# Optimization experiments

Measured on AMD Instinct MI355X. Metric: run time of the kernel, lower is better.

Reference implementation:

```python
import jax, jax.numpy as jnp
import numpy as np

B, H, N, C = 4, 16, 1024, 64
D = H * C  # d_model = 1024


def setup_inputs() -> dict:
    key = jax.random.key(0)
    ks = jax.random.split(key, 6)
    q = jax.random.normal(ks[0], (B, H, N, C), dtype=jnp.float32)
    k = jax.random.normal(ks[1], (B, H, N, C), dtype=jnp.float32)
    v = jax.random.normal(ks[2], (B, H, N, C), dtype=jnp.float32)
    pe = jax.random.normal(ks[3], (1, H, N, N), dtype=jnp.float32)
    # Mlp(h*c): fc1 D->D, SiLU, fc2 D->D (stored as [in, out] for x @ W)
    w1 = jax.random.normal(ks[4], (D, D), dtype=jnp.float32) * (D ** -0.5)
    b1 = jnp.zeros((D,), dtype=jnp.float32)
    w2 = jax.random.normal(ks[5], (D, D), dtype=jnp.float32) * (D ** -0.5)
    b2 = jnp.zeros((D,), dtype=jnp.float32)
    return {"q": q, "k": k, "v": v, "pe": pe,
            "w1": w1, "b1": b1, "w2": w2, "b2": b2}


def reference(q, k, v, pe, w1, b1, w2, b2):
    b, h, n, c = q.shape
    scale = c ** (-0.5)
    # scores: [b,h,n,n]; softmax FIRST, then add pe bias (post-softmax bias)
    scores = jnp.einsum('bhnc,bhmc->bhnm', q, k) * scale
    attn = pe + jax.nn.softmax(scores, axis=-1)
    ctx = jnp.einsum('bhnm,bhmc->bhnc', attn, v)
    # [b,h,n,c] -> [b,n,h*c]
    out = ctx.transpose(0, 2, 1, 3).reshape(b, n, h * c)
    # Mlp: fc1 -> SiLU -> fc2 (dropout is identity at eval)
    hdn = jax.nn.silu(out @ w1 + b1)
    return hdn @ w2 + b2
```

## Files before the change

kernel.cpp:

```cpp
#include <hip/hip_runtime.h>

#define B_ 4
#define H_ 16
#define N_ 1024
#define C_ 64
#define D_ 1024

typedef _Float16 half8 __attribute__((ext_vector_type(8)));
typedef _Float16 half4v __attribute__((ext_vector_type(4)));
typedef float f32x4 __attribute__((ext_vector_type(4)));
typedef float f32x16 __attribute__((ext_vector_type(16)));
typedef unsigned int uint4v __attribute__((ext_vector_type(4)));

#define MFMA16(a, b, c) __builtin_amdgcn_mfma_f32_16x16x32_f16(a, b, c, 0, 0, 0)
#define MFMA32(a, b, c) __builtin_amdgcn_mfma_f32_32x32x16_f16(a, b, c, 0, 0, 0)
#define SM_SHIFT 6.0f

static __device__ __forceinline__ unsigned pk2(float a, float b) {
  auto h = __builtin_amdgcn_cvt_pkrtz(a, b);
  return __builtin_bit_cast(unsigned, h);
}
static __device__ __forceinline__ void swap32(unsigned& a, unsigned& b) {
  asm volatile("v_permlane32_swap_b32 %0, %1" : "+v"(a), "+v"(b));
}
static __device__ __forceinline__ void gload16(const void* g, void* l) {
  __builtin_amdgcn_global_load_lds(
      (const __attribute__((address_space(1))) unsigned int*)g,
      (__attribute__((address_space(3))) unsigned int*)l, 16, 0, 0);
}

__global__ __launch_bounds__(256) void transpose_cvt(
    const float* __restrict__ in, _Float16* __restrict__ outp,
    int in_stride, int out_stride, long in_bstride, long out_bstride)
{
  __shared__ float t[64][65];
  const int tid = threadIdx.x;
  const int r0 = blockIdx.x * 64, c0 = blockIdx.y * 64;
  const float* inb = in + (size_t)blockIdx.z * in_bstride;
  _Float16* outb = outp + (size_t)blockIdx.z * out_bstride;
#pragma unroll
  for (int i = 0; i < 4; ++i) {
    int idx = i * 256 + tid;
    int r = idx >> 4, c4 = (idx & 15) << 2;
    float4 a = *(const float4*)(inb + (size_t)(r0 + r) * in_stride + c0 + c4);
    t[r][c4] = a.x; t[r][c4 + 1] = a.y; t[r][c4 + 2] = a.z; t[r][c4 + 3] = a.w;
  }
  __syncthreads();
#pragma unroll
  for (int i = 0; i < 2; ++i) {
    int idx = i * 256 + tid;
    int rr = idx >> 3, c8 = (idx & 7) << 3;
    half8 hv;
#pragma unroll
    for (int j = 0; j < 8; ++j) hv[j] = (_Float16)t[c8 + j][rr];
    *(half8*)(outb + (size_t)(c0 + rr) * out_stride + r0 + c8) = hv;
  }
}

__global__ __launch_bounds__(512, 1) void pev_kernel(
    const float* __restrict__ pe, const _Float16* __restrict__ vth,
    _Float16* __restrict__ xpe)
{
  __shared__ __align__(16) _Float16 a_lds[2][64][72];
  __shared__ __align__(16) _Float16 b_lds[2][256][72];
  const int tid = threadIdx.x;
  const int n0 = blockIdx.x * 64;
  const int h = blockIdx.y;
  const float* peb = pe + (size_t)h * N_ * N_ + (size_t)n0 * N_;

  const int lane = tid & 63, w = tid >> 6;
  const int l15 = lane & 15, quad = lane >> 4;
  const int wrow = (w >> 2) * 32, wcol = (w & 3) * 64;

  const int ar[2] = { tid >> 4, (512 + tid) >> 4 };
  const int ac4 = (tid & 15) << 2;
  const _Float16* bsrc[4];
  int brow[4], bk8[4];
#pragma unroll
  for (int i = 0; i < 4; ++i) {
    int idx = i * 512 + tid;
    int col = idx >> 3, k8 = (idx & 7) << 3;
    int b = col >> 6, c = col & 63;
    bsrc[i] = vth + ((size_t)(b * H_ + h) * C_ + c) * N_ + k8;
    brow[i] = col;
    bk8[i] = k8;
  }

  f32x4 acc[2][4];
#pragma unroll
  for (int rt = 0; rt < 2; ++rt)
#pragma unroll
    for (int ct = 0; ct < 4; ++ct) acc[rt][ct] = (f32x4){0.f, 0.f, 0.f, 0.f};

  float4 areg[2];
  half8 breg[4];
#pragma unroll
  for (int i = 0; i < 2; ++i) areg[i] = *(const float4*)(peb + (size_t)ar[i] * N_ + ac4);
#pragma unroll
  for (int i = 0; i < 4; ++i) breg[i] = *(const half8*)(bsrc[i]);
#pragma unroll
  for (int i = 0; i < 2; ++i) {
    half4v hv = {(_Float16)areg[i].x, (_Float16)areg[i].y,
                 (_Float16)areg[i].z, (_Float16)areg[i].w};
    *(half4v*)&a_lds[0][ar[i]][ac4] = hv;
  }
#pragma unroll
  for (int i = 0; i < 4; ++i) *(half8*)&b_lds[0][brow[i]][bk8[i]] = breg[i];
#pragma unroll
  for (int i = 0; i < 2; ++i)
    areg[i] = *(const float4*)(peb + (size_t)ar[i] * N_ + 64 + ac4);
#pragma unroll
  for (int i = 0; i < 4; ++i) breg[i] = *(const half8*)(bsrc[i] + 64);
  __syncthreads();

  for (int kt = 0; kt < 16; ++kt) {
    const int cur = kt & 1;
    if (kt < 15) {
#pragma unroll
      for (int i = 0; i < 2; ++i) {
        half4v hv = {(_Float16)areg[i].x, (_Float16)areg[i].y,
                     (_Float16)areg[i].z, (_Float16)areg[i].w};
        *(half4v*)&a_lds[cur ^ 1][ar[i]][ac4] = hv;
      }
#pragma unroll
      for (int i = 0; i < 4; ++i) *(half8*)&b_lds[cur ^ 1][brow[i]][bk8[i]] = breg[i];
    }
    if (kt < 14) {
      int m0 = (kt + 2) * 64;
#pragma unroll
      for (int i = 0; i < 2; ++i)
        areg[i] = *(const float4*)(peb + (size_t)ar[i] * N_ + m0 + ac4);
#pragma unroll
      for (int i = 0; i < 4; ++i) breg[i] = *(const half8*)(bsrc[i] + m0);
    }
#pragma unroll
    for (int s = 0; s < 2; ++s) {
      half8 af[2], bf[4];
#pragma unroll
      for (int rt = 0; rt < 2; ++rt)
        af[rt] = *(const half8*)&a_lds[cur][wrow + rt * 16 + l15][s * 32 + quad * 8];
#pragma unroll
      for (int ct = 0; ct < 4; ++ct)
        bf[ct] = *(const half8*)&b_lds[cur][wcol + ct * 16 + l15][s * 32 + quad * 8];
#pragma unroll
      for (int rt = 0; rt < 2; ++rt)
#pragma unroll
        for (int ct = 0; ct < 4; ++ct)
          acc[rt][ct] = MFMA16(af[rt], bf[ct], acc[rt][ct]);
    }
    __syncthreads();
  }

#pragma unroll
  for (int rt = 0; rt < 2; ++rt)
#pragma unroll
    for (int ct = 0; ct < 4; ++ct) {
      int col = wcol + ct * 16 + l15;
      int b = col >> 6, c = col & 63;
#pragma unroll
      for (int r = 0; r < 4; ++r) {
        int nrow = n0 + wrow + rt * 16 + quad * 4 + r;
        xpe[(size_t)(b * N_ + nrow) * D_ + h * C_ + c] = (_Float16)acc[rt][ct][r];
      }
    }
}

__global__ __launch_bounds__(256, 2) void attn_kernel(
    const float* __restrict__ q, const float* __restrict__ k,
    const _Float16* __restrict__ vth, const _Float16* __restrict__ xpe,
    _Float16* __restrict__ Xh)
{
  __shared__ __align__(16) _Float16 ks[2][2][64][72];
  __shared__ __align__(16) _Float16 vst[2][2][64][72];
  __shared__ float lbuf[128];

  const int tid = threadIdx.x;
  const int bh = blockIdx.x & 63;
  const int qt = blockIdx.x >> 6;
  const int h = bh & (H_ - 1);
  const int b = bh >> 4;
  const int q0 = qt * 128;

  const float* kb = k + (size_t)bh * N_ * C_;
  const _Float16* vb = vth + (size_t)bh * C_ * N_;

  const int lane = tid & 63;
  const int w = tid >> 6;
  const int l31 = lane & 31;
  const int hh = lane >> 5;

  const int sr = tid >> 4, sc4 = (tid & 15) << 2;
  const int vr = tid >> 3, vc8 = (tid & 7) << 3;

  half8 qf[4];
  const float* qrow = q + ((size_t)bh * N_ + q0 + 32 * w + l31) * C_;
#pragma unroll
  for (int sc = 0; sc < 4; ++sc) {
    const float* qp = qrow + 16 * sc + 8 * hh;
    float4 t0 = *(const float4*)qp;
    float4 t1 = *(const float4*)(qp + 4);
    half8 hv = { (_Float16)(t0.x * 0.125f), (_Float16)(t0.y * 0.125f),
                 (_Float16)(t0.z * 0.125f), (_Float16)(t0.w * 0.125f),
                 (_Float16)(t1.x * 0.125f), (_Float16)(t1.y * 0.125f),
                 (_Float16)(t1.z * 0.125f), (_Float16)(t1.w * 0.125f) };
    qf[sc] = hv;
  }

  f32x16 Os2[2];
  Os2[0] = (f32x16)(0.f); Os2[1] = (f32x16)(0.f);
  float l4[4] = {0.f, 0.f, 0.f, 0.f};

  float4 kreg[8];
  uint4 vreg[4];

#pragma unroll
  for (int s = 0; s < 2; ++s) {
#pragma unroll
    for (int i = 0; i < 4; ++i)
      kreg[s * 4 + i] = *(const float4*)(kb + (size_t)(s * 64 + sr + i * 16) * C_ + sc4);
#pragma unroll
    for (int i = 0; i < 2; ++i)
      vreg[s * 2 + i] = *(const uint4*)(vb + (size_t)(vr + i * 32) * N_ + s * 64 + vc8);
  }
#pragma unroll
  for (int s = 0; s < 2; ++s) {
#pragma unroll
    for (int i = 0; i < 4; ++i) {
      float4 kv = kreg[s * 4 + i];
      half4v hk = {(_Float16)kv.x, (_Float16)kv.y, (_Float16)kv.z, (_Float16)kv.w};
      *(half4v*)&ks[0][s][sr + i * 16][sc4] = hk;
    }
#pragma unroll
    for (int i = 0; i < 2; ++i) *(uint4*)&vst[0][s][vr + i * 32][vc8] = vreg[s * 2 + i];
  }
#pragma unroll
  for (int s = 0; s < 2; ++s) {
#pragma unroll
    for (int i = 0; i < 4; ++i)
      kreg[s * 4 + i] = *(const float4*)(kb + (size_t)(128 + s * 64 + sr + i * 16) * C_ + sc4);
#pragma unroll
    for (int i = 0; i < 2; ++i)
      vreg[s * 2 + i] = *(const uint4*)(vb + (size_t)(vr + i * 32) * N_ + 128 + s * 64 + vc8);
  }
  __syncthreads();

  for (int p = 0; p < 8; ++p) {
    const int cur = p & 1;
    if (p < 7) {
#pragma unroll
      for (int s = 0; s < 2; ++s) {
#pragma unroll
        for (int i = 0; i < 4; ++i) {
          float4 kv = kreg[s * 4 + i];
          half4v hk = {(_Float16)kv.x, (_Float16)kv.y, (_Float16)kv.z, (_Float16)kv.w};
          *(half4v*)&ks[cur ^ 1][s][sr + i * 16][sc4] = hk;
        }
#pragma unroll
        for (int i = 0; i < 2; ++i)
          *(uint4*)&vst[cur ^ 1][s][vr + i * 32][vc8] = vreg[s * 2 + i];
      }
    }
    if (p < 6) {
      int m0 = (p + 2) * 128;
#pragma unroll
      for (int s = 0; s < 2; ++s) {
#pragma unroll
        for (int i = 0; i < 4; ++i)
          kreg[s * 4 + i] = *(const float4*)(kb + (size_t)(m0 + s * 64 + sr + i * 16) * C_ + sc4);
#pragma unroll
        for (int i = 0; i < 2; ++i)
          vreg[s * 2 + i] = *(const uint4*)(vb + (size_t)(vr + i * 32) * N_ + m0 + s * 64 + vc8);
      }
    }

    half8 pa[2][4];
#pragma unroll
    for (int s = 0; s < 2; ++s) {
      f32x16 sacc2[2];
      sacc2[0] = (f32x16)(0.f); sacc2[1] = (f32x16)(0.f);
#pragma unroll
      for (int sc = 0; sc < 4; ++sc) {
        half8 ak0 = *(const half8*)&ks[cur][s][l31][16 * sc + 8 * hh];
        half8 ak1 = *(const half8*)&ks[cur][s][32 + l31][16 * sc + 8 * hh];
        sacc2[0] = MFMA32(ak0, qf[sc], sacc2[0]);
        sacc2[1] = MFMA32(ak1, qf[sc], sacc2[1]);
      }
#pragma unroll
      for (int kbt = 0; kbt < 2; ++kbt) {
        float pv[16];
#pragma unroll
        for (int r = 0; r < 16; ++r) {
          pv[r] = __expf(sacc2[kbt][r] - SM_SHIFT);
          l4[r & 3] += pv[r];
        }
#pragma unroll
        for (int sp = 0; sp < 2; ++sp) {
          const int rb = 8 * sp;
          unsigned wa = pk2(pv[rb + 0], pv[rb + 1]);
          unsigned wb = pk2(pv[rb + 4], pv[rb + 5]);
          unsigned wc = pk2(pv[rb + 2], pv[rb + 3]);
          unsigned wd = pk2(pv[rb + 6], pv[rb + 7]);
          swap32(wa, wb);
          swap32(wc, wd);
          uint4v pw = {wa, wc, wb, wd};
          pa[s][kbt * 2 + sp] = __builtin_bit_cast(half8, pw);
        }
      }
    }

#pragma unroll
    for (int s = 0; s < 2; ++s)
#pragma unroll
      for (int st = 0; st < 4; ++st) {
        half8 bv0 = *(const half8*)&vst[cur][s][l31][16 * st + 8 * hh];
        half8 bv1 = *(const half8*)&vst[cur][s][32 + l31][16 * st + 8 * hh];
        Os2[0] = MFMA32(pa[s][st], bv0, Os2[0]);
        Os2[1] = MFMA32(pa[s][st], bv1, Os2[1]);
      }

    __syncthreads();
  }

  float l = (l4[0] + l4[1]) + (l4[2] + l4[3]);
  l += __shfl_xor(l, 32);
  lbuf[32 * w + l31] = 1.0f / l;

#pragma unroll
  for (int reg = 0; reg < 16; ++reg) {
    const int qi = (reg & 3) + 8 * (reg >> 2) + 4 * hh;
    const float li = lbuf[32 * w + qi];
    const size_t row = (size_t)(b * N_ + q0 + 32 * w + qi);
#pragma unroll
    for (int ct = 0; ct < 2; ++ct) {
      size_t o = row * D_ + h * C_ + 32 * ct + l31;
      Xh[o] = (_Float16)(Os2[ct][reg] * li + (float)xpe[o]);
    }
  }
}

template <bool SILU, typename OT>
__global__ __launch_bounds__(256, 2) void mlp_kernel(
    const _Float16* __restrict__ X, const _Float16* __restrict__ Wt,
    const float* __restrict__ bias, OT* __restrict__ Y)
{
  __shared__ __align__(16) _Float16 a_lds[3][128 * 64];
  __shared__ __align__(16) _Float16 b_lds[3][64 * 64];
  const int tid = threadIdx.x;
  const int id = blockIdx.x;
  const int xcd = id & 7, j = id >> 3;
  const int m0 = (xcd * 4 + (j & 3)) * 128;
  const int n0 = (j >> 2) * 64;
  const int lane = tid & 63, w = tid >> 6;
  const int wr = (w >> 1) * 64, wc = (w & 1) * 32;
  const int l15 = lane & 15, quad = lane >> 4;

  const int lrow8 = lane >> 3;
  const int lg = lane & 7;

  f32x4 acc[4][2];
#pragma unroll
  for (int rt = 0; rt < 4; ++rt)
#pragma unroll
    for (int ct = 0; ct < 2; ++ct) acc[rt][ct] = (f32x4){0.f, 0.f, 0.f, 0.f};

#define STAGE_MLP(buf, k0)                                                     \
  {                                                                            \
    int ar0 = w * 32;                                                          \
    int br0 = w * 16;                                                          \
    for (int jj = 0; jj < 4; ++jj) {                                           \
      int r = ar0 + jj * 8 + lrow8;                                            \
      const _Float16* src = X + (size_t)(m0 + r) * D_ + (k0) + ((lg ^ (r & 7)) << 3); \
      gload16(src, &a_lds[buf][(ar0 + jj * 8) * 64]);                          \
    }                                                                          \
    for (int jj = 0; jj < 2; ++jj) {                                           \
      int r = br0 + jj * 8 + lrow8;                                            \
      const _Float16* src = Wt + (size_t)(n0 + r) * D_ + (k0) + ((lg ^ (r & 7)) << 3); \
      gload16(src, &b_lds[buf][(br0 + jj * 8) * 64]);                          \
    }                                                                          \
  }

  STAGE_MLP(0, 0);
  STAGE_MLP(1, 64);

  for (int kt = 0; kt < 16; ++kt) {
    const int cur = kt % 3;
    if (kt < 15) asm volatile("s_waitcnt vmcnt(6)" ::: "memory");
    else         asm volatile("s_waitcnt vmcnt(0)" ::: "memory");
    __builtin_amdgcn_sched_barrier(0);
    __builtin_amdgcn_s_barrier();
    if (kt < 14) {
      const int nb = (kt + 2) % 3;
      STAGE_MLP(nb, (kt + 2) * 64);
    }
#pragma unroll
    for (int s = 0; s < 2; ++s) {
      half8 af[4], bf[2];
#pragma unroll
      for (int rt = 0; rt < 4; ++rt) {
        int row = wr + rt * 16 + l15;
        af[rt] = *(const half8*)&a_lds[cur][row * 64 + (((s * 4 + quad) ^ (row & 7)) << 3)];
      }
#pragma unroll
      for (int ct = 0; ct < 2; ++ct) {
        int row = wc + ct * 16 + l15;
        bf[ct] = *(const half8*)&b_lds[cur][row * 64 + (((s * 4 + quad) ^ (row & 7)) << 3)];
      }
#pragma unroll
      for (int rt = 0; rt < 4; ++rt)
#pragma unroll
        for (int ct = 0; ct < 2; ++ct)
          acc[rt][ct] = MFMA16(af[rt], bf[ct], acc[rt][ct]);
    }
  }
#undef STAGE_MLP

  float bv[2];
#pragma unroll
  for (int ct = 0; ct < 2; ++ct) bv[ct] = bias[n0 + wc + ct * 16 + l15];
#pragma unroll
  for (int rt = 0; rt < 4; ++rt)
#pragma unroll
    for (int ct = 0; ct < 2; ++ct)
#pragma unroll
      for (int r = 0; r < 4; ++r) {
        float val = acc[rt][ct][r] + bv[ct];
        if (SILU) val = val / (1.f + __expf(-val));
        int row = m0 + wr + rt * 16 + quad * 4 + r;
        int col = n0 + wc + ct * 16 + l15;
        Y[(size_t)row * D_ + col] = (OT)val;
      }
}

extern "C" void kernel_launch(void* const* d_in, const int* in_sizes, int n_in,
                              void* d_out, int out_size, void* d_ws, size_t ws_size,
                              hipStream_t stream) {
  const float* q  = (const float*)d_in[0];
  const float* k  = (const float*)d_in[1];
  const float* v  = (const float*)d_in[2];
  const float* pe = (const float*)d_in[3];
  const float* w1 = (const float*)d_in[4];
  const float* b1 = (const float*)d_in[5];
  const float* w2 = (const float*)d_in[6];
  const float* b2 = (const float*)d_in[7];
  float* out = (float*)d_out;

  _Float16* Xh  = (_Float16*)d_out;
  _Float16* vth = (_Float16*)((char*)d_out + (size_t)8 * 1024 * 1024);
  _Float16* xpeH1 = (_Float16*)d_ws;
  _Float16* w1t = (_Float16*)((char*)d_ws + (size_t)8 * 1024 * 1024);
  _Float16* w2t = (_Float16*)((char*)d_ws + (size_t)10 * 1024 * 1024);

  transpose_cvt<<<dim3(16, 16, 1), 256, 0, stream>>>(w1, w1t, D_, D_, 0, 0);
  transpose_cvt<<<dim3(16, 16, 1), 256, 0, stream>>>(w2, w2t, D_, D_, 0, 0);
  transpose_cvt<<<dim3(16, 1, B_ * H_), 256, 0, stream>>>(
      v, vth, C_, N_, (long)N_ * C_, (long)N_ * C_);
  pev_kernel<<<dim3(N_ / 64, H_), 512, 0, stream>>>(pe, vth, xpeH1);
  attn_kernel<<<dim3(B_ * H_ * (N_ / 128)), 256, 0, stream>>>(q, k, vth, xpeH1, Xh);
  mlp_kernel<true, _Float16><<<dim3(512), 256, 0, stream>>>(Xh, w1t, b1, xpeH1);
  mlp_kernel<false, float><<<dim3(512), 256, 0, stream>>>(xpeH1, w2t, b2, out);
}
```

Baseline: 244.1 us.

## Stream V tiles via async global-to-LDS loads with XOR swizzle and priority hints

V tiles are now copied straight from global memory into a swizzled LDS buffer with asynchronous global_load_lds, replacing the register round-trip and ds_write staging. The end-of-iteration sync becomes a manual vmcnt/lgkmcnt wait plus s_barrier, so the K register prefetch can stay in flight. The softmax switches to exp2 with a log2e-folded Q scale, and s_setprio raises wave priority around the MFMA blocks. The hand-written waitcnt counts depend on how many loads are outstanding, so a mismatch could cause races.

```diff
diff --git a/kernel.cpp b/kernel.cpp
--- a/kernel.cpp
+++ b/kernel.cpp
@@ -14,7 +14,8 @@
 
 #define MFMA16(a, b, c) __builtin_amdgcn_mfma_f32_16x16x32_f16(a, b, c, 0, 0, 0)
 #define MFMA32(a, b, c) __builtin_amdgcn_mfma_f32_32x32x16_f16(a, b, c, 0, 0, 0)
-#define SM_SHIFT 6.0f
+#define QSCALE 0.18033688011112042f
+#define SM_SHIFT2 8.656170245333781f
 
 static __device__ __forceinline__ unsigned pk2(float a, float b) {
   auto h = __builtin_amdgcn_cvt_pkrtz(a, b);
@@ -171,7 +172,7 @@
     _Float16* __restrict__ Xh)
 {
   __shared__ __align__(16) _Float16 ks[2][2][64][72];
-  __shared__ __align__(16) _Float16 vst[2][2][64][72];
+  __shared__ __align__(16) _Float16 vl[2][64][128];
   __shared__ float lbuf[128];
 
   const int tid = threadIdx.x;
@@ -190,7 +191,21 @@
   const int hh = lane >> 5;
 
   const int sr = tid >> 4, sc4 = (tid & 15) << 2;
-  const int vr = tid >> 3, vc8 = (tid & 7) << 3;
+
+  const int vrow4 = lane >> 4;
+  const int vg = lane & 15;
+  const int vsw = l31 & 15;
+
+#define STAGE_V(buf, koff)                                                     \
+  {                                                                            \
+    _Pragma("unroll")                                                          \
+    for (int jj = 0; jj < 4; ++jj) {                                           \
+      const int rbase = w * 16 + jj * 4;                                       \
+      const int r = rbase + vrow4;                                             \
+      const _Float16* src = vb + (size_t)r * N_ + (koff) + ((vg ^ (r & 15)) << 3); \
+      gload16(src, &vl[buf][rbase][0]);                                        \
+    }                                                                          \
+  }
 
   half8 qf[4];
   const float* qrow = q + ((size_t)bh * N_ + q0 + 32 * w + l31) * C_;
@@ -199,10 +214,10 @@
     const float* qp = qrow + 16 * sc + 8 * hh;
     float4 t0 = *(const float4*)qp;
     float4 t1 = *(const float4*)(qp + 4);
-    half8 hv = { (_Float16)(t0.x * 0.125f), (_Float16)(t0.y * 0.125f),
-                 (_Float16)(t0.z * 0.125f), (_Float16)(t0.w * 0.125f),
-                 (_Float16)(t1.x * 0.125f), (_Float16)(t1.y * 0.125f),
-                 (_Float16)(t1.z * 0.125f), (_Float16)(t1.w * 0.125f) };
+    half8 hv = { (_Float16)(t0.x * QSCALE), (_Float16)(t0.y * QSCALE),
+                 (_Float16)(t0.z * QSCALE), (_Float16)(t0.w * QSCALE),
+                 (_Float16)(t1.x * QSCALE), (_Float16)(t1.y * QSCALE),
+                 (_Float16)(t1.z * QSCALE), (_Float16)(t1.w * QSCALE) };
     qf[sc] = hv;
   }
 
@@ -211,19 +226,15 @@
   float l4[4] = {0.f, 0.f, 0.f, 0.f};
 
   float4 kreg[8];
-  uint4 vreg[4];
-
-#pragma unroll
-  for (int s = 0; s < 2; ++s) {
+
+  STAGE_V(0, 0);
+#pragma unroll
+  for (int s = 0; s < 2; ++s)
 #pragma unroll
     for (int i = 0; i < 4; ++i)
       kreg[s * 4 + i] = *(const float4*)(kb + (size_t)(s * 64 + sr + i * 16) * C_ + sc4);
 #pragma unroll
-    for (int i = 0; i < 2; ++i)
-      vreg[s * 2 + i] = *(const uint4*)(vb + (size_t)(vr + i * 32) * N_ + s * 64 + vc8);
-  }
-#pragma unroll
-  for (int s = 0; s < 2; ++s) {
+  for (int s = 0; s < 2; ++s)
 #pragma unroll
     for (int i = 0; i < 4; ++i) {
       float4 kv = kreg[s * 4 + i];
@@ -231,46 +242,33 @@
       *(half4v*)&ks[0][s][sr + i * 16][sc4] = hk;
     }
 #pragma unroll
-    for (int i = 0; i < 2; ++i) *(uint4*)&vst[0][s][vr + i * 32][vc8] = vreg[s * 2 + i];
-  }
-#pragma unroll
-  for (int s = 0; s < 2; ++s) {
+  for (int s = 0; s < 2; ++s)
 #pragma unroll
     for (int i = 0; i < 4; ++i)
       kreg[s * 4 + i] = *(const float4*)(kb + (size_t)(128 + s * 64 + sr + i * 16) * C_ + sc4);
-#pragma unroll
-    for (int i = 0; i < 2; ++i)
-      vreg[s * 2 + i] = *(const uint4*)(vb + (size_t)(vr + i * 32) * N_ + 128 + s * 64 + vc8);
-  }
   __syncthreads();
 
   for (int p = 0; p < 8; ++p) {
     const int cur = p & 1;
+    if (p < 7) STAGE_V(cur ^ 1, (p + 1) * 128);
+    __builtin_amdgcn_sched_barrier(0);
     if (p < 7) {
 #pragma unroll
-      for (int s = 0; s < 2; ++s) {
+      for (int s = 0; s < 2; ++s)
 #pragma unroll
         for (int i = 0; i < 4; ++i) {
           float4 kv = kreg[s * 4 + i];
           half4v hk = {(_Float16)kv.x, (_Float16)kv.y, (_Float16)kv.z, (_Float16)kv.w};
           *(half4v*)&ks[cur ^ 1][s][sr + i * 16][sc4] = hk;
         }
-#pragma unroll
-        for (int i = 0; i < 2; ++i)
-          *(uint4*)&vst[cur ^ 1][s][vr + i * 32][vc8] = vreg[s * 2 + i];
-      }
     }
     if (p < 6) {
       int m0 = (p + 2) * 128;
 #pragma unroll
-      for (int s = 0; s < 2; ++s) {
+      for (int s = 0; s < 2; ++s)
 #pragma unroll
         for (int i = 0; i < 4; ++i)
           kreg[s * 4 + i] = *(const float4*)(kb + (size_t)(m0 + s * 64 + sr + i * 16) * C_ + sc4);
-#pragma unroll
-        for (int i = 0; i < 2; ++i)
-          vreg[s * 2 + i] = *(const uint4*)(vb + (size_t)(vr + i * 32) * N_ + m0 + s * 64 + vc8);
-      }
     }
 
     half8 pa[2][4];
@@ -278,6 +276,7 @@
     for (int s = 0; s < 2; ++s) {
       f32x16 sacc2[2];
       sacc2[0] = (f32x16)(0.f); sacc2[1] = (f32x16)(0.f);
+      __builtin_amdgcn_s_setprio(1);
 #pragma unroll
       for (int sc = 0; sc < 4; ++sc) {
         half8 ak0 = *(const half8*)&ks[cur][s][l31][16 * sc + 8 * hh];
@@ -285,12 +284,13 @@
         sacc2[0] = MFMA32(ak0, qf[sc], sacc2[0]);
         sacc2[1] = MFMA32(ak1, qf[sc], sacc2[1]);
       }
+      __builtin_amdgcn_s_setprio(0);
 #pragma unroll
       for (int kbt = 0; kbt < 2; ++kbt) {
         float pv[16];
 #pragma unroll
         for (int r = 0; r < 16; ++r) {
-          pv[r] = __expf(sacc2[kbt][r] - SM_SHIFT);
+          pv[r] = exp2f(sacc2[kbt][r] - SM_SHIFT2);
           l4[r & 3] += pv[r];
         }
 #pragma unroll
@@ -308,18 +308,28 @@
       }
     }
 
+    __builtin_amdgcn_s_setprio(1);
 #pragma unroll
     for (int s = 0; s < 2; ++s)
 #pragma unroll
       for (int st = 0; st < 4; ++st) {
-        half8 bv0 = *(const half8*)&vst[cur][s][l31][16 * st + 8 * hh];
-        half8 bv1 = *(const half8*)&vst[cur][s][32 + l31][16 * st + 8 * hh];
+        const int gv = s * 8 + st * 2 + hh;
+        half8 bv0 = *(const half8*)&vl[cur][l31][(gv ^ vsw) << 3];
+        half8 bv1 = *(const half8*)&vl[cur][32 + l31][(gv ^ vsw) << 3];
         Os2[0] = MFMA32(pa[s][st], bv0, Os2[0]);
         Os2[1] = MFMA32(pa[s][st], bv1, Os2[1]);
       }
-
-    __syncthreads();
-  }
+    __builtin_amdgcn_s_setprio(0);
+
+    if (p < 7) {
+      __builtin_amdgcn_sched_barrier(0);
+      if (p < 6) asm volatile("s_waitcnt vmcnt(8) lgkmcnt(0)" ::: "memory");
+      else       asm volatile("s_waitcnt vmcnt(0) lgkmcnt(0)" ::: "memory");
+      __builtin_amdgcn_sched_barrier(0);
+      __builtin_amdgcn_s_barrier();
+    }
+  }
+#undef STAGE_V
 
   float l = (l4[0] + l4[1]) + (l4[2] + l4[3]);
   l += __shfl_xor(l, 32);
```

Result: no change. 239.9 us (-1.7%).
